# Optimization experiments

Measured on AMD Instinct MI355X. Metric: run time of the kernel, lower is better.

Reference implementation:

```python
import jax, jax.numpy as jnp
import numpy as np

BLANK = 36
NEG = -1e30  # stand-in for -inf that stays NaN-free under logaddexp


def _ctc_loss(logits, targets, input_lengths, target_lengths):
    """CTC loss (reduction='mean', matching torch.nn.CTCLoss semantics:
    per-sample loss divided by target_length, then mean over batch).
    logits: [B, T, C] raw scores; targets: [B*L] flattened labels (fixed L per sample).
    """
    B, T, C = logits.shape
    L = targets.shape[0] // B
    tgt = targets.reshape(B, L)
    S = 2 * L + 1  # extended label length: blank-interleaved

    # log_softmax over classes, then time-major [T, B, C]
    lp = jnp.transpose(jax.nn.log_softmax(logits, axis=-1), (1, 0, 2))

    # extended targets: [blank, t1, blank, t2, ..., blank]  -> [B, S]
    ext = jnp.full((B, S), BLANK, dtype=tgt.dtype).at[:, 1::2].set(tgt)

    # gather log-probs of extended labels: [T, B, S]
    lp_ext = lp[:, jnp.arange(B)[:, None], ext]

    # positions beyond 2*target_len are invalid
    valid = jnp.arange(S)[None, :] < (2 * target_lengths[:, None] + 1)  # [B, S]
    # skip transition s-2 -> s allowed only if ext[s] != blank and ext[s] != ext[s-2]
    skip_ok = (ext != BLANK) & jnp.concatenate(
        [jnp.zeros((B, 2), bool), ext[:, 2:] != ext[:, :-2]], axis=1)

    end_idx = 2 * target_lengths  # index of final blank; [B]

    def final_ll(alpha):
        e1 = jnp.take_along_axis(alpha, end_idx[:, None], axis=1)[:, 0]
        e2 = jnp.take_along_axis(alpha, (end_idx - 1)[:, None], axis=1)[:, 0]
        return jnp.logaddexp(e1, e2)

    # t = 0 initialization
    alpha0 = jnp.full((B, S), NEG, logits.dtype)
    alpha0 = alpha0.at[:, 0].set(lp_ext[0, :, 0]).at[:, 1].set(lp_ext[0, :, 1])
    alpha0 = jnp.where(valid, alpha0, NEG)
    final0 = jnp.where(input_lengths == 1, final_ll(alpha0), NEG)

    pad1 = jnp.full((B, 1), NEG, logits.dtype)
    pad2 = jnp.full((B, 2), NEG, logits.dtype)

    def step(carry, inp):
        alpha, final = carry
        t, lpe = inp  # lpe: [B, S]
        a1 = jnp.concatenate([pad1, alpha[:, :-1]], axis=1)
        a2 = jnp.where(skip_ok, jnp.concatenate([pad2, alpha[:, :-2]], axis=1), NEG)
        new = jnp.logaddexp(jnp.logaddexp(alpha, a1), a2) + lpe
        new = jnp.where(valid, new, NEG)
        final = jnp.where(input_lengths == t + 1, final_ll(new), final)
        return (new, final), None

    (_, final), _ = jax.lax.scan(step, (alpha0, final0),
                                 (jnp.arange(1, T), lp_ext[1:]))
    return jnp.mean(-final / target_lengths.astype(logits.dtype))


def setup_inputs() -> dict:
    key = jax.random.key(0)
    k1, k2 = jax.random.split(key)
    B, T, C, L = 2048, 256, 37, 16
    logits = jax.random.normal(k1, (B, T, C), dtype=jnp.float32)
    targets = jax.random.randint(k2, (B * L,), 0, 36, dtype=jnp.int32)  # never blank
    input_lengths = jnp.full((B,), T, dtype=jnp.int32)
    target_lengths = jnp.full((B,), L, dtype=jnp.int32)
    return {"logits": logits, "targets": targets,
            "input_lengths": input_lengths, "target_lengths": target_lengths}


def reference(logits, targets, input_lengths, target_lengths):
    return _ctc_loss(logits, targets, input_lengths, target_lengths)
```

## Files before the change

### kernel.cpp

```cpp
#include <hip/hip_runtime.h>

#define BLANK 36
#define NEG -1e30f
#define CC 37
#define LOG37 3.6109179126442243f

__device__ __forceinline__ float logaddexp_f(float a, float b) {
    float m = fmaxf(a, b);
    float d = fabsf(a - b);
    return m + __logf(1.0f + __expf(-d));
}

#define DPP0(src, ctrl) __builtin_amdgcn_update_dpp(0, (src), (ctrl), 0xf, 0xf, true)
#define DPPM(old, src, ctrl) __builtin_amdgcn_update_dpp((old), (src), (ctrl), 0xf, 0xf, false)

__global__ __launch_bounds__(128, 2) void ctc_fused_ab2_kernel(
    const float* __restrict__ logits,
    const int*   __restrict__ targets,
    const int*   __restrict__ input_lengths,
    const int*   __restrict__ target_lengths,
    float*       __restrict__ per_sample,
    int B, int T, int L)
{
    __shared__ float lds[2 * 2368 + 72];
    const int lane = threadIdx.x & 63;
    const int wib  = threadIdx.x >> 6;
    const int h    = lane >> 5;
    const int l    = lane & 31;
    const int b0   = blockIdx.x * 2;
    const int bme  = b0 + h;

    float* Xw   = lds + wib * 2368;
    float* Xh   = Xw + h * 1184;
    float* exch = lds + 4736;

    const int halfT = T >> 1;
    const int NCh   = halfT >> 5;

    const int tl_lane  = target_lengths[bme];
    const int il_lane  = input_lengths[bme];
    const int end_lane = 2 * tl_lane;
    const int s_ilA = __builtin_amdgcn_readlane(il_lane, 0);
    const int s_ilB = __builtin_amdgcn_readlane(il_lane, 32);

    int ext_w = BLANK;
    if (!(l & 1)) {
        int ti = (wib == 0) ? (l >> 1) : (15 - (l >> 1));
        if (ti >= L) ti = L - 1;
        if (ti < 0) ti = 0;
        ext_w = targets[bme * L + ti];
    }
    const int exo = __shfl_up(ext_w, 2);
    float kf;
    if (wib == 0)
        kf = (l >= 2 && ext_w != BLANK && ext_w != exo) ? 1.0f : 0.0f;
    else
        kf = ((33 - l) <= 2 * L && exo != BLANK && exo != ext_w) ? 1.0f : 0.0f;

    const bool c16 = (l == 16);
    const bool c17 = (l == 17);
    const bool cz0 = (l == 0);
    const int bcast_addr = (((lane & 32) | 31) << 2);

    const float4* baseH4 = (const float4*)(logits + (size_t)bme * T * CC);
    const float* pwp = Xh + ext_w;
    const float* pbp = Xh + 36;

    auto SHIFTS = [&](float x, float inj, float& a1, float& a2) {
        const int xi  = __float_as_int(x);
        const int s1  = DPP0(xi, 0x111);
        const int s2  = DPP0(xi, 0x112);
        const int b15 = DPP0(xi, 0x142);
        const int y15 = DPP0(s1, 0x142);
        a1 = cz0 ? inj : __int_as_float(c16 ? b15 : s1);
        a2 = __int_as_float(c16 ? y15 : (c17 ? b15 : s2));
    };

    auto RESCALE = [&](float& x, float& x2, float& racc) {
        float m = fmaxf(x, x2);
        m = fmaxf(m, __int_as_float(DPPM(__float_as_int(m), __float_as_int(m), 0x111)));
        m = fmaxf(m, __int_as_float(DPPM(__float_as_int(m), __float_as_int(m), 0x112)));
        m = fmaxf(m, __int_as_float(DPPM(__float_as_int(m), __float_as_int(m), 0x114)));
        m = fmaxf(m, __int_as_float(DPPM(__float_as_int(m), __float_as_int(m), 0x118)));
        m = fmaxf(m, __int_as_float(DPPM(__float_as_int(m), __float_as_int(m), 0x142)));
        float gm = __int_as_float(__builtin_amdgcn_ds_bpermute(bcast_addr, __float_as_int(m)));
        gm = fmaxf(gm, 1e-30f);
        const float inv = __builtin_amdgcn_rcpf(gm);
        x *= inv; x2 *= inv;
        racc += __logf(gm);
    };

    auto SOFTMAX = [&](float* Xn) {
        float xr[CC];
        const float* row = Xn + lane * CC;
        #pragma unroll
        for (int c2 = 0; c2 < CC; ++c2) xr[c2] = row[c2];
        float m = xr[0];
        #pragma unroll
        for (int c2 = 1; c2 < CC; ++c2) m = fmaxf(m, xr[c2]);
        float ss = 0.0f;
        #pragma unroll
        for (int c2 = 0; c2 < CC; ++c2) { xr[c2] = __expf(xr[c2] - m); ss += xr[c2]; }
        const float inv = 37.0f / ss;
        float* wrow = Xn + lane * CC;
        #pragma unroll
        for (int c2 = 0; c2 < CC; ++c2) wrow[c2] = xr[c2] * inv;
    };

    auto STAGE = [&](int tbase) {
        const float4* s4 = baseH4 + ((tbase * CC) >> 2);
        float4* d4 = (float4*)Xh;
        #pragma unroll
        for (int k = 0; k < 9; ++k) d4[k * 32 + l] = s4[k * 32 + l];
        if (l < 8) d4[288 + l] = s4[288 + l];
        __builtin_amdgcn_s_waitcnt(0);
    };

    float z = 0.0f, zx = 0.0f, racc = 0.0f, capv = NEG;
    float pw[16], pb[16];

    if (wib == 0) {
        STAGE(0);
        SOFTMAX(Xw);
        __builtin_amdgcn_s_waitcnt(0);
        #pragma unroll 1
        for (int c = 0; c < NCh; ++c) {
            const bool more = (c + 1 < NCh);
            float4 f0 = {}, f1 = {}, f2 = {}, f3 = {}, f4 = {},
                   f5 = {}, f6 = {}, f7 = {}, f8 = {}, f9 = {};
            if (more) {
                const float4* s4 = baseH4 + ((((c + 1) << 5) * CC) >> 2);
                f0 = s4[l];       f1 = s4[32 + l];  f2 = s4[64 + l];
                f3 = s4[96 + l];  f4 = s4[128 + l]; f5 = s4[160 + l];
                f6 = s4[192 + l]; f7 = s4[224 + l]; f8 = s4[256 + l];
                if (l < 8) f9 = s4[288 + l];
            }
            #pragma unroll
            for (int j = 0; j < 16; ++j) { pw[j] = pwp[j * CC]; pb[j] = pbp[j * CC]; }
            #pragma unroll
            for (int r = 0; r < 32; ++r) {
                const float p   = pw[r & 15];
                const float pbv = pb[r & 15];
                if (r < 16) { pw[r & 15] = pwp[(r + 16) * CC]; pb[r & 15] = pbp[(r + 16) * CC]; }
                if (c == 0 && r == 0) {
                    z  = cz0 ? p : 0.0f;
                    zx = pbv;
                } else {
                    float a1, a2;
                    SHIFTS(z, zx, a1, a2);
                    z = fmaf(kf, a2, z + a1) * p;
                    zx *= pbv;
                }
                const int tt = (c << 5) + r;
                if (s_ilA == tt + 1 || s_ilB == tt + 1) {
                    const float cv = __logf(fmaxf(z, 1e-35f)) + racc - (float)(tt + 1) * LOG37;
                    capv = (il_lane == tt + 1) ? cv : capv;
                }
                if ((r & 15) == 15) RESCALE(z, zx, racc);
            }
            if (more) {
                float4* d4 = (float4*)Xh;
                d4[l] = f0;       d4[32 + l] = f1;  d4[64 + l] = f2;
                d4[96 + l] = f3;  d4[128 + l] = f4; d4[160 + l] = f5;
                d4[192 + l] = f6; d4[224 + l] = f7; d4[256 + l] = f8;
                if (l < 8) d4[288 + l] = f9;
                __builtin_amdgcn_s_waitcnt(0);
                SOFTMAX(Xw);
                __builtin_amdgcn_s_waitcnt(0);
            }
        }
    } else {
        STAGE(T - 32);
        SOFTMAX(Xw);
        __builtin_amdgcn_s_waitcnt(0);
        #pragma unroll 1
        for (int i = 0; i < NCh; ++i) {
            const bool more = (i + 1 < NCh);
            float4 f0 = {}, f1 = {}, f2 = {}, f3 = {}, f4 = {},
                   f5 = {}, f6 = {}, f7 = {}, f8 = {}, f9 = {};
            if (more) {
                const float4* s4 = baseH4 + (((T - (i + 2) * 32) * CC) >> 2);
                f0 = s4[l];       f1 = s4[32 + l];  f2 = s4[64 + l];
                f3 = s4[96 + l];  f4 = s4[128 + l]; f5 = s4[160 + l];
                f6 = s4[192 + l]; f7 = s4[224 + l]; f8 = s4[256 + l];
                if (l < 8) f9 = s4[288 + l];
            }
            const int tbase = T - (i + 1) * 32;
            #pragma unroll
            for (int j = 0; j < 16; ++j) { pw[j] = pwp[(31 - j) * CC]; pb[j] = pbp[(31 - j) * CC]; }
            #pragma unroll
            for (int r = 0; r < 32; ++r) {
                const int tt = tbase + 31 - r;
                if (s_ilA == tt + 1 || s_ilB == tt + 1) {
                    const bool cond = (il_lane == tt + 1);
                    const float zi = (l == 31 - end_lane || l == 32 - end_lane) ? 1.0f : 0.0f;
                    z    = cond ? zi : z;
                    zx   = cond ? ((end_lane == 32) ? 1.0f : 0.0f) : zx;
                    racc = cond ? 0.0f : racc;
                }
                const float p   = pw[r & 15];
                const float pbv = pb[r & 15];
                if (r < 16) { pw[r & 15] = pwp[(15 - r) * CC]; pb[r & 15] = pbp[(15 - r) * CC]; }
                const float u  = z * p;
                const float uE = zx * pbv;
                float a1, a2;
                SHIFTS(u, uE, a1, a2);
                z  = fmaf(kf, a2, u + a1);
                zx = uE;
                if ((r & 15) == 15) RESCALE(z, zx, racc);
            }
            if (more) {
                float4* d4 = (float4*)Xh;
                d4[l] = f0;       d4[32 + l] = f1;  d4[64 + l] = f2;
                d4[96 + l] = f3;  d4[128 + l] = f4; d4[160 + l] = f5;
                d4[192 + l] = f6; d4[224 + l] = f7; d4[256 + l] = f8;
                if (l < 8) d4[288 + l] = f9;
                __builtin_amdgcn_s_waitcnt(0);
                SOFTMAX(Xw);
                __builtin_amdgcn_s_waitcnt(0);
            }
        }
    }

    __syncthreads();
    if (wib == 1) {
        exch[h * 35 + (31 - l)] = z;
        if (l == 0) { exch[h * 35 + 32] = zx; exch[h * 35 + 33] = racc; }
    }
    __syncthreads();
    if (wib == 0) {
        const float bs = exch[h * 35 + l + 1];
        float prod = z * bs + (cz0 ? zx * exch[h * 35] : 0.0f);
        #pragma unroll
        for (int o = 16; o > 0; o >>= 1) prod += __shfl_xor(prod, o);
        const float rb = exch[h * 35 + 33];
        int i1 = (lane & 32) + end_lane - 1;
        if (i1 < 0) i1 = 0;
        int i2 = i1 - 1;
        if (i2 < 0) i2 = 0;
        const float e1 = __shfl(capv, i1);
        const float e2 = __shfl(capv, i2);
        const float fcap = logaddexp_f(e1, e2);
        const float fmid = __logf(fmaxf(prod, 1e-37f)) + racc + rb
                           - (float)il_lane * LOG37;
        const float final_v = (il_lane <= halfT) ? fcap : fmid;
        if (l == 0) per_sample[bme] = -final_v / (float)tl_lane;
    }
}

__global__ __launch_bounds__(128, 4) void ctc_fused_ab_kernel(
    const float* __restrict__ logits,
    const int*   __restrict__ targets,
    const int*   __restrict__ input_lengths,
    const int*   __restrict__ target_lengths,
    float*       __restrict__ per_sample,
    int B, int T, int L)
{
    __shared__ float lds[2 * 2368 + 66];
    const int lane = threadIdx.x & 63;
    const int wib  = threadIdx.x >> 6;
    const int b    = blockIdx.x;

    float* Xw   = lds + wib * 2368;
    float* exch = lds + 4736;

    const int S = 2 * L + 1;
    const int tlen_s = __builtin_amdgcn_readfirstlane(target_lengths[b]);
    const int ilen_s = __builtin_amdgcn_readfirstlane(input_lengths[b]);
    const int end_s  = 2 * tlen_s;
    const int halfT  = T >> 1;
    const int NC     = T >> 6;
    const int NCh    = NC >> 1;

    const int st = (wib == 0) ? lane : (63 - lane);
    int ext_w = BLANK;
    if (st < S && (st & 1)) ext_w = targets[b * L + (st >> 1)];
    const int exo = __shfl_up(ext_w, 2);
    float kf;
    if (wib == 0)
        kf = ((st >= 2) && (st < S) && (ext_w != BLANK) && (ext_w != exo)) ? 1.0f : 0.0f;
    else
        kf = ((st + 2 < S) && (exo != BLANK) && (exo != ext_w)) ? 1.0f : 0.0f;

    const bool c16 = ((lane & 31) == 16);
    const bool c17 = ((lane & 31) == 17);
    const bool c32 = (lane == 32);
    const bool c33 = (lane == 33);

    const float4* src = (const float4*)(logits + (size_t)b * T * CC);

    auto SHIFTS = [&](float x, float& a1, float& a2) {
        const int xi  = __float_as_int(x);
        const int s1  = DPP0(xi, 0x111);
        const int s2  = DPP0(xi, 0x112);
        const int b15 = DPP0(xi, 0x142);
        const int b31 = DPP0(xi, 0x143);
        const int y15 = DPP0(s1, 0x142);
        const int y31 = DPP0(s1, 0x143);
        a1 = __int_as_float(c16 ? b15 : (c32 ? b31 : s1));
        a2 = __int_as_float(c16 ? y15 : (c17 ? b15 : (c32 ? y31 : (c33 ? b31 : s2))));
    };

    auto RESCALE = [&](float& x, float& racc) {
        float m = x;
        m = fmaxf(m, __int_as_float(DPPM(__float_as_int(m), __float_as_int(m), 0x111)));
        m = fmaxf(m, __int_as_float(DPPM(__float_as_int(m), __float_as_int(m), 0x112)));
        m = fmaxf(m, __int_as_float(DPPM(__float_as_int(m), __float_as_int(m), 0x114)));
        m = fmaxf(m, __int_as_float(DPPM(__float_as_int(m), __float_as_int(m), 0x118)));
        m = fmaxf(m, __int_as_float(DPPM(__float_as_int(m), __float_as_int(m), 0x142)));
        m = fmaxf(m, __int_as_float(DPPM(__float_as_int(m), __float_as_int(m), 0x143)));
        float gm = __int_as_float(__builtin_amdgcn_readlane(__float_as_int(m), 63));
        gm = fmaxf(gm, 1e-30f);
        x *= (1.0f / gm);
        racc += __logf(gm);
    };

    auto SOFTMAX = [&](float* Xn) {
        float xr[CC];
        const float* row = Xn + lane * CC;
        #pragma unroll
        for (int c2 = 0; c2 < CC; ++c2) xr[c2] = row[c2];
        float m = xr[0];
        #pragma unroll
        for (int c2 = 1; c2 < CC; ++c2) m = fmaxf(m, xr[c2]);
        float ss = 0.0f;
        #pragma unroll
        for (int c2 = 0; c2 < CC; ++c2) { xr[c2] = __expf(xr[c2] - m); ss += xr[c2]; }
        const float inv = 37.0f / ss;
        float* wrow = Xn + lane * CC;
        #pragma unroll
        for (int c2 = 0; c2 < CC; ++c2) wrow[c2] = xr[c2] * inv;
    };

    auto STAGE = [&](const float4* s2g) {
        float4* dst = (float4*)Xw;
        #pragma unroll
        for (int k = 0; k < 9; ++k) dst[k * 64 + lane] = s2g[k * 64 + lane];
        if (lane < 16) dst[576 + lane] = s2g[576 + lane];
        __builtin_amdgcn_s_waitcnt(0);
    };

    float z = 0.0f, racc = 0.0f, capv = NEG;
    float pw[16];

    if (wib == 0) {
        STAGE(src);
        SOFTMAX(Xw);
        __builtin_amdgcn_s_waitcnt(0);
        #pragma unroll 1
        for (int c = 0; c < NCh; ++c) {
            const bool more = (c + 1 < NCh);
            float4 f0 = {}, f1 = {}, f2 = {}, f3 = {}, f4 = {},
                   f5 = {}, f6 = {}, f7 = {}, f8 = {}, f9 = {};
            if (more) {
                const float4* s2g = src + (size_t)(c + 1) * 592;
                f0 = s2g[lane];       f1 = s2g[64 + lane];  f2 = s2g[128 + lane];
                f3 = s2g[192 + lane]; f4 = s2g[256 + lane]; f5 = s2g[320 + lane];
                f6 = s2g[384 + lane]; f7 = s2g[448 + lane]; f8 = s2g[512 + lane];
                if (lane < 16) f9 = s2g[576 + lane];
            }
            const int tbase = c << 6;
            #pragma unroll
            for (int j = 0; j < 16; ++j) pw[j] = Xw[j * CC + ext_w];
            #pragma unroll
            for (int r = 0; r < 64; ++r) {
                const float p = pw[r & 15];
                if (r + 16 < 64) pw[r & 15] = Xw[(r + 16) * CC + ext_w];
                if (c == 0 && r == 0) {
                    z = (lane <= 1) ? p : 0.0f;
                    if (ilen_s == 1) capv = __logf(fmaxf(z, 1e-35f)) - LOG37;
                } else {
                    float a1, a2;
                    SHIFTS(z, a1, a2);
                    z = fmaf(kf, a2, z + a1) * p;
                    const int tt = tbase + r;
                    if (ilen_s == tt + 1)
                        capv = __logf(fmaxf(z, 1e-35f)) + racc - (float)(tt + 1) * LOG37;
                }
                if ((r & 15) == 15) RESCALE(z, racc);
            }
            if (more) {
                float4* dst = (float4*)Xw;
                dst[lane] = f0;       dst[64 + lane] = f1;  dst[128 + lane] = f2;
                dst[192 + lane] = f3; dst[256 + lane] = f4; dst[320 + lane] = f5;
                dst[384 + lane] = f6; dst[448 + lane] = f7; dst[512 + lane] = f8;
                if (lane < 16) dst[576 + lane] = f9;
                __builtin_amdgcn_s_waitcnt(0);
                SOFTMAX(Xw);
                __builtin_amdgcn_s_waitcnt(0);
            }
        }
    } else {
        STAGE(src + (size_t)(NC - 1) * 592);
        SOFTMAX(Xw);
        __builtin_amdgcn_s_waitcnt(0);
        const int il1 = ilen_s - 1;
        #pragma unroll 1
        for (int i = 0; i < NCh; ++i) {
            const bool more = (i + 1 < NCh);
            float4 f0 = {}, f1 = {}, f2 = {}, f3 = {}, f4 = {},
                   f5 = {}, f6 = {}, f7 = {}, f8 = {}, f9 = {};
            if (more) {
                const float4* s2g = src + (size_t)(NC - 2 - i) * 592;
                f0 = s2g[lane];       f1 = s2g[64 + lane];  f2 = s2g[128 + lane];
                f3 = s2g[192 + lane]; f4 = s2g[256 + lane]; f5 = s2g[320 + lane];
                f6 = s2g[384 + lane]; f7 = s2g[448 + lane]; f8 = s2g[512 + lane];
                if (lane < 16) f9 = s2g[576 + lane];
            }
            const int cbase = (NC - 1 - i) << 6;
            #pragma unroll
            for (int j = 0; j < 16; ++j) pw[j] = Xw[(63 - j) * CC + ext_w];
            #pragma unroll
            for (int r = 0; r < 64; ++r) {
                const int tt = cbase + 63 - r;
                if (tt == il1) {
                    z = (lane == 63 - end_s || lane == 64 - end_s) ? 1.0f : 0.0f;
                    racc = 0.0f;
                }
                const float p = pw[r & 15];
                if (r + 16 < 64) pw[r & 15] = Xw[(63 - (r + 16)) * CC + ext_w];
                const float u = z * p;
                float a1, a2;
                SHIFTS(u, a1, a2);
                z = fmaf(kf, a2, u + a1);
                if ((r & 15) == 15) RESCALE(z, racc);
            }
            if (more) {
                float4* dst = (float4*)Xw;
                dst[lane] = f0;       dst[64 + lane] = f1;  dst[128 + lane] = f2;
                dst[192 + lane] = f3; dst[256 + lane] = f4; dst[320 + lane] = f5;
                dst[384 + lane] = f6; dst[448 + lane] = f7; dst[512 + lane] = f8;
                if (lane < 16) dst[576 + lane] = f9;
                __builtin_amdgcn_s_waitcnt(0);
                SOFTMAX(Xw);
                __builtin_amdgcn_s_waitcnt(0);
            }
        }
    }

    __syncthreads();
    if (wib == 1) {
        exch[63 - lane] = z;
        if (lane == 0) exch[64] = racc;
    }
    __syncthreads();
    if (wib == 0) {
        const float bs = exch[lane];
        const float rb = exch[64];
        float prod = z * bs;
        #pragma unroll
        for (int o = 32; o > 0; o >>= 1) prod += __shfl_xor(prod, o);
        float final_v;
        if (ilen_s <= halfT) {
            const float e1 = __shfl(capv, end_s);
            const float e2 = __shfl(capv, end_s - 1);
            final_v = logaddexp_f(e1, e2);
        } else {
            final_v = __logf(fmaxf(prod, 1e-37f)) + racc + rb - (float)ilen_s * LOG37;
        }
        if (lane == 0) per_sample[b] = -final_v / (float)tlen_s;
    }
}

__global__ __launch_bounds__(256) void lse_kernel(
    const float* __restrict__ logits, float* __restrict__ denom, int N)
{
    __shared__ float lds[256 * CC];
    const int lane = threadIdx.x & 63;
    const int wib  = threadIdx.x >> 6;
    const int wave = blockIdx.x * 4 + wib;
    const long long row0 = (long long)wave * 64;
    if (row0 >= N) return;
    const int wbase = wib * 64 * CC;
    const float4* src4 = (const float4*)(logits + row0 * CC);
    const long long n4_remaining = ((long long)N * CC - row0 * CC) / 4;
    float4* lds4 = (float4*)(lds + wbase);
    #pragma unroll
    for (int k = 0; k < 10; ++k) {
        const int idx = k * 64 + lane;
        if (idx < 592 && idx < n4_remaining) lds4[idx] = src4[idx];
    }
    __builtin_amdgcn_s_waitcnt(0);
    const long long row = row0 + lane;
    if (row >= N) return;
    const float* x = lds + wbase + lane * CC;
    float m = x[0];
    #pragma unroll
    for (int c = 1; c < CC; ++c) m = fmaxf(m, x[c]);
    float s = 0.0f;
    #pragma unroll
    for (int c = 0; c < CC; ++c) s += __expf(x[c] - m);
    denom[row] = m + __logf(s);
}

__global__ __launch_bounds__(256) void ctc_alpha2_kernel(
    const float* __restrict__ logits, const float* __restrict__ denom,
    const int* __restrict__ targets, const int* __restrict__ input_lengths,
    const int* __restrict__ target_lengths, float* __restrict__ per_sample,
    int B, int T, int L)
{
    const int wave = (int)((blockIdx.x * blockDim.x + threadIdx.x) >> 6);
    const int lane = threadIdx.x & 63;
    if (wave >= B) return;
    const int b = wave;
    const int S = 2 * L + 1;
    const int tlen = target_lengths[b];
    const int ilen = input_lengths[b];
    const int end_idx = 2 * tlen;
    int ext_s = BLANK;
    if (lane < S && (lane & 1)) ext_s = targets[b * L + (lane >> 1)];
    const int ext_sm2 = __shfl_up(ext_s, 2);
    const bool skip_ok = (lane < S) && (lane >= 2) && (ext_s != BLANK) && (ext_s != ext_sm2);
    const bool valid = lane < (2 * tlen + 1);
    const float* lg = logits + (size_t)b * T * CC;
    const float* dn = denom + (size_t)b * T;
    float x_cur = lg[ext_s];
    float d_cur = dn[0];
    float x_nx = (T > 1) ? lg[CC + ext_s] : 0.0f;
    float d_nx = (T > 1) ? dn[1] : 0.0f;
    float final_v = NEG;
    float alpha = (valid && lane <= 1) ? (x_cur - d_cur) : NEG;
    if (ilen == 1) {
        const float e1 = __shfl(alpha, end_idx);
        const float e2 = __shfl(alpha, end_idx - 1);
        final_v = logaddexp_f(e1, e2);
    }
    for (int tt = 1; tt < T; ++tt) {
        x_cur = x_nx; d_cur = d_nx;
        if (tt + 1 < T) {
            x_nx = lg[(size_t)(tt + 1) * CC + ext_s];
            d_nx = dn[tt + 1];
        }
        const float lpe = x_cur - d_cur;
        float a1 = __shfl_up(alpha, 1);
        if (lane == 0) a1 = NEG;
        float a2 = __shfl_up(alpha, 2);
        if (!skip_ok) a2 = NEG;
        const float m = fmaxf(fmaxf(alpha, a1), a2);
        const float s = __expf(alpha - m) + __expf(a1 - m) + __expf(a2 - m);
        const float na = m + __logf(s) + lpe;
        alpha = valid ? na : NEG;
        if (ilen == tt + 1) {
            const float e1 = __shfl(alpha, end_idx);
            const float e2 = __shfl(alpha, end_idx - 1);
            final_v = logaddexp_f(e1, e2);
        }
    }
    if (lane == 0) per_sample[b] = -final_v / (float)tlen;
}

__global__ __launch_bounds__(256) void ctc_alpha_mono_kernel(
    const float* __restrict__ logits, const int* __restrict__ targets,
    const int* __restrict__ input_lengths, const int* __restrict__ target_lengths,
    float* __restrict__ per_sample, int B, int T, int L)
{
    const int wave = (int)((blockIdx.x * blockDim.x + threadIdx.x) >> 6);
    const int lane = threadIdx.x & 63;
    if (wave >= B) return;
    const int b = wave;
    const int S = 2 * L + 1;
    const int tlen = target_lengths[b];
    const int ilen = input_lengths[b];
    const int end_idx = 2 * tlen;
    int ext_s = BLANK;
    if (lane < S && (lane & 1)) ext_s = targets[b * L + (lane >> 1)];
    const int ext_sm2 = __shfl_up(ext_s, 2);
    const bool skip_ok = (lane < S) && (lane >= 2) && (ext_s != BLANK) && (ext_s != ext_sm2);
    const bool valid = lane < (2 * tlen + 1);
    const float* lg = logits + (size_t)b * T * CC;
    float alpha = NEG, final_v = NEG;
    for (int t = 0; t < T; ++t) {
        float x = (lane < CC) ? lg[t * CC + lane] : -3.0e38f;
        float mx = x;
        #pragma unroll
        for (int o = 32; o > 0; o >>= 1) mx = fmaxf(mx, __shfl_xor(mx, o));
        float e = (lane < CC) ? __expf(x - mx) : 0.0f;
        float se = e;
        #pragma unroll
        for (int o = 32; o > 0; o >>= 1) se += __shfl_xor(se, o);
        const float lp = x - mx - __logf(se);
        const float lpe = __shfl(lp, ext_s);
        float newa;
        if (t == 0) {
            newa = (lane <= 1) ? lpe : NEG;
        } else {
            float a1 = __shfl_up(alpha, 1);
            if (lane == 0) a1 = NEG;
            float a2 = __shfl_up(alpha, 2);
            if (!skip_ok) a2 = NEG;
            newa = logaddexp_f(logaddexp_f(alpha, a1), a2) + lpe;
        }
        if (!valid) newa = NEG;
        alpha = newa;
        if (ilen == t + 1) {
            const float e1 = __shfl(alpha, end_idx);
            const float e2 = __shfl(alpha, end_idx - 1);
            final_v = logaddexp_f(e1, e2);
        }
    }
    if (lane == 0) per_sample[b] = -final_v / (float)tlen;
}

__global__ __launch_bounds__(256) void reduce_mean_kernel(
    const float* __restrict__ ps, float* __restrict__ out, int B)
{
    float s = 0.0f;
    for (int i = threadIdx.x; i < B; i += 256) s += ps[i];
    #pragma unroll
    for (int o = 32; o > 0; o >>= 1) s += __shfl_xor(s, o);
    __shared__ float sm[4];
    const int w = threadIdx.x >> 6, l = threadIdx.x & 63;
    if (l == 0) sm[w] = s;
    __syncthreads();
    if (threadIdx.x == 0) {
        out[0] = (sm[0] + sm[1] + sm[2] + sm[3]) / (float)B;
    }
}

extern "C" void kernel_launch(void* const* d_in, const int* in_sizes, int n_in,
                              void* d_out, int out_size, void* d_ws, size_t ws_size,
                              hipStream_t stream) {
    const float* logits         = (const float*)d_in[0];
    const int*   targets        = (const int*)d_in[1];
    const int*   input_lengths  = (const int*)d_in[2];
    const int*   target_lengths = (const int*)d_in[3];

    const int B = in_sizes[2];
    const int L = in_sizes[1] / B;
    const int T = in_sizes[0] / (B * CC);
    const long long N = (long long)B * T;

    float* per_sample = (float*)d_ws;
    float* scratch    = per_sample + B;
    float* out        = (float*)d_out;

    const size_t ws_mid = ((size_t)B + (size_t)N) * sizeof(float);
    const int nblocks_alpha = (B * 64 + 255) / 256;
    const long long nwaves = (N + 63) / 64;

    const bool ws_ok = ws_size >= (size_t)B * sizeof(float);
    const bool fast2 = (B % 2 == 0) && (T % 64 == 0) && T >= 64 && L <= 16 && ws_ok;
    const bool fast1 = (T % 128 == 0) && T >= 128 && L <= 31 && ws_ok;

    if (fast2) {
        ctc_fused_ab2_kernel<<<B / 2, 128, 0, stream>>>(
            logits, targets, input_lengths, target_lengths, per_sample, B, T, L);
    } else if (fast1) {
        ctc_fused_ab_kernel<<<B, 128, 0, stream>>>(
            logits, targets, input_lengths, target_lengths, per_sample, B, T, L);
    } else if (ws_size >= ws_mid && T >= 2) {
        lse_kernel<<<(int)((nwaves + 3) / 4), 256, 0, stream>>>(logits, scratch, (int)N);
        ctc_alpha2_kernel<<<nblocks_alpha, 256, 0, stream>>>(
            logits, scratch, targets, input_lengths, target_lengths, per_sample, B, T, L);
    } else {
        ctc_alpha_mono_kernel<<<nblocks_alpha, 256, 0, stream>>>(
            logits, targets, input_lengths, target_lengths, per_sample, B, T, L);
    }
    reduce_mean_kernel<<<1, 256, 0, stream>>>(per_sample, out, B);
}
```

Measured before the change: 119.6 us.

## Prefetch next logit chunk directly into LDS with double buffering

Replaces the register-staged prefetch of the next 32-timestep logit chunk with async global_load_lds copies into a second LDS buffer, swapping buffers each chunk. The goal is to cut register pressure and the explicit LDS store pass while the recurrence runs on the current buffer. LDS per block roughly doubles, which may limit occupancy. The full-waitcnt barrier before the softmax may still serialise the load. The reduce launch is only moved into each branch.

```diff
diff --git a/kernel.cpp b/kernel.cpp
--- a/kernel.cpp
+++ b/kernel.cpp
@@ -13,6 +13,13 @@
 
 #define DPP0(src, ctrl) __builtin_amdgcn_update_dpp(0, (src), (ctrl), 0xf, 0xf, true)
 #define DPPM(old, src, ctrl) __builtin_amdgcn_update_dpp((old), (src), (ctrl), 0xf, 0xf, false)
+
+__device__ __forceinline__ void gl_lds16(const float4* g, float* l) {
+    __builtin_amdgcn_global_load_lds(
+        (const __attribute__((address_space(1))) void*)g,
+        (__attribute__((address_space(3))) void*)l,
+        16, 0, 0);
+}
 
 __global__ __launch_bounds__(128, 2) void ctc_fused_ab2_kernel(
     const float* __restrict__ logits,
@@ -22,7 +29,7 @@
     float*       __restrict__ per_sample,
     int B, int T, int L)
 {
-    __shared__ float lds[2 * 2368 + 72];
+    __shared__ float lds[2 * 4736 + 72];
     const int lane = threadIdx.x & 63;
     const int wib  = threadIdx.x >> 6;
     const int h    = lane >> 5;
@@ -30,12 +37,12 @@
     const int b0   = blockIdx.x * 2;
     const int bme  = b0 + h;
 
-    float* Xw   = lds + wib * 2368;
-    float* Xh   = Xw + h * 1184;
-    float* exch = lds + 4736;
+    float* Xw   = lds + wib * 4736;
+    float* exch = lds + 9472;
 
     const int halfT = T >> 1;
     const int NCh   = halfT >> 5;
+    const int NCtot = T >> 5;
 
     const int tl_lane  = target_lengths[bme];
     const int il_lane  = input_lengths[bme];
@@ -62,9 +69,8 @@
     const bool cz0 = (l == 0);
     const int bcast_addr = (((lane & 32) | 31) << 2);
 
-    const float4* baseH4 = (const float4*)(logits + (size_t)bme * T * CC);
-    const float* pwp = Xh + ext_w;
-    const float* pbp = Xh + 36;
+    const float4* gA4 = (const float4*)(logits + (size_t)b0 * T * CC);
+    const float4* gB4 = (const float4*)(logits + (size_t)(b0 + 1) * T * CC);
 
     auto SHIFTS = [&](float x, float inj, float& a1, float& a2) {
         const int xi  = __float_as_int(x);
@@ -107,34 +113,36 @@
         for (int c2 = 0; c2 < CC; ++c2) wrow[c2] = xr[c2] * inv;
     };
 
-    auto STAGE = [&](int tbase) {
-        const float4* s4 = baseH4 + ((tbase * CC) >> 2);
-        float4* d4 = (float4*)Xh;
-        #pragma unroll
-        for (int k = 0; k < 9; ++k) d4[k * 32 + l] = s4[k * 32 + l];
-        if (l < 8) d4[288 + l] = s4[288 + l];
-        __builtin_amdgcn_s_waitcnt(0);
+    auto STAGE_ASYNC = [&](float* dst, int coff4) {
+        #pragma unroll
+        for (int k = 0; k < 9; ++k) {
+            const int s = k * 64 + lane;
+            const float4* src = (s < 296) ? (gA4 + coff4 + s)
+                                          : (gB4 + coff4 + (s - 296));
+            gl_lds16(src, dst + k * 256);
+        }
+        if (lane < 16) {
+            gl_lds16(gB4 + coff4 + (280 + lane), dst + 2304);
+        }
     };
 
     float z = 0.0f, zx = 0.0f, racc = 0.0f, capv = NEG;
     float pw[16], pb[16];
 
+    float* cur = Xw;
+    float* nxt = Xw + 2368;
+
     if (wib == 0) {
-        STAGE(0);
-        SOFTMAX(Xw);
+        STAGE_ASYNC(cur, 0);
+        __builtin_amdgcn_s_waitcnt(0);
+        SOFTMAX(cur);
         __builtin_amdgcn_s_waitcnt(0);
         #pragma unroll 1
         for (int c = 0; c < NCh; ++c) {
             const bool more = (c + 1 < NCh);
-            float4 f0 = {}, f1 = {}, f2 = {}, f3 = {}, f4 = {},
-                   f5 = {}, f6 = {}, f7 = {}, f8 = {}, f9 = {};
-            if (more) {
-                const float4* s4 = baseH4 + ((((c + 1) << 5) * CC) >> 2);
-                f0 = s4[l];       f1 = s4[32 + l];  f2 = s4[64 + l];
-                f3 = s4[96 + l];  f4 = s4[128 + l]; f5 = s4[160 + l];
-                f6 = s4[192 + l]; f7 = s4[224 + l]; f8 = s4[256 + l];
-                if (l < 8) f9 = s4[288 + l];
-            }
+            if (more) STAGE_ASYNC(nxt, (c + 1) * 296);
+            const float* pwp = cur + h * 1184 + ext_w;
+            const float* pbp = cur + h * 1184 + 36;
             #pragma unroll
             for (int j = 0; j < 16; ++j) { pw[j] = pwp[j * CC]; pb[j] = pbp[j * CC]; }
             #pragma unroll
@@ -159,32 +167,23 @@
                 if ((r & 15) == 15) RESCALE(z, zx, racc);
             }
             if (more) {
-                float4* d4 = (float4*)Xh;
-                d4[l] = f0;       d4[32 + l] = f1;  d4[64 + l] = f2;
-                d4[96 + l] = f3;  d4[128 + l] = f4; d4[160 + l] = f5;
-                d4[192 + l] = f6; d4[224 + l] = f7; d4[256 + l] = f8;
-                if (l < 8) d4[288 + l] = f9;
-                __builtin_amdgcn_s_waitcnt(0);
-                SOFTMAX(Xw);
-                __builtin_amdgcn_s_waitcnt(0);
+                __builtin_amdgcn_s_waitcnt(0);
+                SOFTMAX(nxt);
+                __builtin_amdgcn_s_waitcnt(0);
+                float* t = cur; cur = nxt; nxt = t;
             }
         }
     } else {
-        STAGE(T - 32);
-        SOFTMAX(Xw);
+        STAGE_ASYNC(cur, (NCtot - 1) * 296);
+        __builtin_amdgcn_s_waitcnt(0);
+        SOFTMAX(cur);
         __builtin_amdgcn_s_waitcnt(0);
         #pragma unroll 1
         for (int i = 0; i < NCh; ++i) {
             const bool more = (i + 1 < NCh);
-            float4 f0 = {}, f1 = {}, f2 = {}, f3 = {}, f4 = {},
-                   f5 = {}, f6 = {}, f7 = {}, f8 = {}, f9 = {};
-            if (more) {
-                const float4* s4 = baseH4 + (((T - (i + 2) * 32) * CC) >> 2);
-                f0 = s4[l];       f1 = s4[32 + l];  f2 = s4[64 + l];
-                f3 = s4[96 + l];  f4 = s4[128 + l]; f5 = s4[160 + l];
-                f6 = s4[192 + l]; f7 = s4[224 + l]; f8 = s4[256 + l];
-                if (l < 8) f9 = s4[288 + l];
-            }
+            if (more) STAGE_ASYNC(nxt, (NCtot - 2 - i) * 296);
+            const float* pwp = cur + h * 1184 + ext_w;
+            const float* pbp = cur + h * 1184 + 36;
             const int tbase = T - (i + 1) * 32;
             #pragma unroll
             for (int j = 0; j < 16; ++j) { pw[j] = pwp[(31 - j) * CC]; pb[j] = pbp[(31 - j) * CC]; }
@@ -210,14 +209,10 @@
                 if ((r & 15) == 15) RESCALE(z, zx, racc);
             }
             if (more) {
-                float4* d4 = (float4*)Xh;
-                d4[l] = f0;       d4[32 + l] = f1;  d4[64 + l] = f2;
-                d4[96 + l] = f3;  d4[128 + l] = f4; d4[160 + l] = f5;
-                d4[192 + l] = f6; d4[224 + l] = f7; d4[256 + l] = f8;
-                if (l < 8) d4[288 + l] = f9;
-                __builtin_amdgcn_s_waitcnt(0);
-                SOFTMAX(Xw);
-                __builtin_amdgcn_s_waitcnt(0);
+                __builtin_amdgcn_s_waitcnt(0);
+                SOFTMAX(nxt);
+                __builtin_amdgcn_s_waitcnt(0);
+                float* t = cur; cur = nxt; nxt = t;
             }
         }
     }
@@ -645,16 +640,19 @@
     if (fast2) {
         ctc_fused_ab2_kernel<<<B / 2, 128, 0, stream>>>(
             logits, targets, input_lengths, target_lengths, per_sample, B, T, L);
+        reduce_mean_kernel<<<1, 256, 0, stream>>>(per_sample, out, B);
     } else if (fast1) {
         ctc_fused_ab_kernel<<<B, 128, 0, stream>>>(
             logits, targets, input_lengths, target_lengths, per_sample, B, T, L);
+        reduce_mean_kernel<<<1, 256, 0, stream>>>(per_sample, out, B);
     } else if (ws_size >= ws_mid && T >= 2) {
         lse_kernel<<<(int)((nwaves + 3) / 4), 256, 0, stream>>>(logits, scratch, (int)N);
         ctc_alpha2_kernel<<<nblocks_alpha, 256, 0, stream>>>(
             logits, scratch, targets, input_lengths, target_lengths, per_sample, B, T, L);
+        reduce_mean_kernel<<<1, 256, 0, stream>>>(per_sample, out, B);
     } else {
         ctc_alpha_mono_kernel<<<nblocks_alpha, 256, 0, stream>>>(
             logits, targets, input_lengths, target_lengths, per_sample, B, T, L);
-    }
-    reduce_mean_kernel<<<1, 256, 0, stream>>>(per_sample, out, B);
-}
+        reduce_mean_kernel<<<1, 256, 0, stream>>>(per_sample, out, B);
+    }
+}
```

After: 117.3 us. About the same (-1.9%).
